# Kernel optimization log

Hardware: AMD Instinct MI355X
Metric: run time of the kernel (lower is better)

## Reference

```python
import jax, jax.numpy as jnp
import numpy as np

E, S, L, V, PMAX = 256, 64, 3, 256, 2000
DILATIONS = (1, 2, 4, 8)


def _layernorm(x, g, b, eps=1e-5):
    m = x.mean(-1, keepdims=True)
    v = ((x - m) ** 2).mean(-1, keepdims=True)
    return (x - m) * jax.lax.rsqrt(v + eps) * g + b


def _ssm_layer(x, in_w, conv_w, conv_b, dt_w, A_log, D_param, B_w, C_w, out_w, ln_g, ln_b):
    # x: [B, T, D]
    Bsz, T, Dm = x.shape
    xr = x @ in_w.T                                  # [B,T,2D]
    x_in, x_res = xr[..., :Dm], xr[..., Dm:]
    # causal depthwise conv, kernel=4, left-pad 3 (== torch pad=3 then [:, :, :T])
    xt = x_in.transpose(0, 2, 1)                     # [B,D,T]
    xc = jax.lax.conv_general_dilated(
        xt, conv_w[:, None, :], (1,), [(3, 0)],
        feature_group_count=Dm, dimension_numbers=('NCH', 'OIH', 'NCH'))
    xc = jax.nn.silu((xc + conv_b[None, :, None]).transpose(0, 2, 1))  # [B,T,D]
    A = -jnp.exp(A_log)                              # [D,S]
    Bm = xc @ B_w.T                                  # [B,T,S]
    Cm = xc @ C_w.T                                  # [B,T,S]
    dt = jax.nn.softplus(dt_w)                       # [D] per-channel timestep
    dA = 1.0 + dt[:, None] * A                       # Euler discretization I + dt*A, [D,S]
    h0 = jnp.zeros((Bsz, Dm, S), x.dtype)

    def step(h, inp):
        u_t, B_t, C_t = inp                          # [B,D],[B,S],[B,S]
        h = dA * h + (dt * u_t)[:, :, None] * B_t[:, None, :]   # [B,D,S]
        y = jnp.einsum('bs,bds->bd', C_t, h)
        return h, y

    _, ys = jax.lax.scan(step, h0, (xc.transpose(1, 0, 2), Bm.transpose(1, 0, 2), Cm.transpose(1, 0, 2)))
    y = ys.transpose(1, 0, 2) + D_param * xc         # [B,T,D]
    y = (y * jax.nn.silu(x_res)) @ out_w.T
    return _layernorm(y + x, ln_g, ln_b)


def _forward(tokens, tok_emb, pos_emb, in_w, conv_w, conv_b, dt_w, A_log, D_param,
             B_w, C_w, out_w, ln_g, ln_b, ctx_w, ctx_b, fus_w, fus_b, fus_ln_g, fus_ln_b):
    Bsz, T = tokens.shape
    x = tok_emb[tokens] + pos_emb[:T][None]          # [B,T,E]
    feats = x
    for i in range(L):
        feats = _ssm_layer(feats, in_w[i], conv_w[i], conv_b[i], dt_w[i], A_log[i],
                           D_param[i], B_w[i], C_w[i], out_w[i], ln_g[i], ln_b[i])
    # multi-dilation context convs on the raw embeddings
    xt = x.transpose(0, 2, 1)                        # [B,E,T]
    ctx = []
    for j, d in enumerate(DILATIONS):
        o = jax.lax.conv_general_dilated(
            xt, ctx_w[j], (1,), [(d, d)], rhs_dilation=(d,),
            dimension_numbers=('NCH', 'OIH', 'NCH'))
        ctx.append(o + ctx_b[j][None, :, None])
    ctx = jnp.concatenate(ctx, axis=1).transpose(0, 2, 1)      # [B,T,E]
    fused = jax.nn.relu(jnp.concatenate([feats, ctx], -1) @ fus_w.T + fus_b)
    return _layernorm(fused, fus_ln_g, fus_ln_b)


def setup_inputs() -> dict:
    key = jax.random.key(0)
    ks = jax.random.split(key, 16)
    Bsz, T = 32, 2000

    def n(k, shape, s):
        return jax.random.normal(k, shape, jnp.float32) * s

    return {
        'tokens': jax.random.randint(ks[0], (Bsz, T), 0, V),
        'tok_emb': n(ks[1], (V, E), 1.0),
        'pos_emb': n(ks[2], (PMAX, E), 1.0),
        'in_w': n(ks[3], (L, 2 * E, E), 0.05),
        'conv_w': n(ks[4], (L, E, 4), 0.2),
        'conv_b': jnp.zeros((L, E), jnp.float32),
        'dt_w': jax.random.uniform(ks[5], (L, E), jnp.float32, -0.01, 0.01),
        'A_log': jax.random.uniform(ks[6], (L, E, S), jnp.float32, -4.0, -1.0),
        'D_param': jnp.zeros((L, E), jnp.float32),
        'B_w': n(ks[7], (L, S, E), 0.05),
        'C_w': n(ks[8], (L, S, E), 0.05),
        'out_w': n(ks[9], (L, E, E), 0.05),
        'ln_g': jnp.ones((L, E), jnp.float32),
        'ln_b': jnp.zeros((L, E), jnp.float32),
        'ctx_w': n(ks[10], (4, E // 4, E, 3), 0.05),
        'ctx_b': jnp.zeros((4, E // 4), jnp.float32),
        'fus_w': n(ks[11], (E, 2 * E), 0.05),
        'fus_b': jnp.zeros((E,), jnp.float32),
        'fus_ln_g': jnp.ones((E,), jnp.float32),
        'fus_ln_b': jnp.zeros((E,), jnp.float32),
    }


def reference(tokens, tok_emb, pos_emb, in_w, conv_w, conv_b, dt_w, A_log, D_param,
              B_w, C_w, out_w, ln_g, ln_b, ctx_w, ctx_b, fus_w, fus_b, fus_ln_g, fus_ln_b):
    return _forward(tokens, tok_emb, pos_emb, in_w, conv_w, conv_b, dt_w, A_log, D_param,
                    B_w, C_w, out_w, ln_g, ln_b, ctx_w, ctx_b, fus_w, fus_b, fus_ln_g, fus_ln_b)
```

## Files before the change

### kernel.cpp

```cpp
#include <hip/hip_runtime.h>
#include <stdint.h>

#define B_ 32
#define T_ 2000
#define E_ 256
#define S_ 64
#define L_ 3
#define BT_ (B_*T_)
#define NC_ 25
#define CL_ 80
#define TS_ 16
#define NT_ (CL_/TS_)
#define TP_ (T_+16)

typedef short s8v __attribute__((ext_vector_type(8)));
typedef short s4v __attribute__((ext_vector_type(4)));
typedef float f4v __attribute__((ext_vector_type(4)));
typedef float f2v __attribute__((ext_vector_type(2)));
typedef unsigned short us;

__device__ __forceinline__ float b2f(us u){
    return __uint_as_float(((unsigned int)u) << 16);
}
__device__ __forceinline__ us f2b(float f){
    unsigned int x = __float_as_uint(f);
    x += 0x7fffu + ((x >> 16) & 1u);
    return (us)(x >> 16);
}

__global__ __launch_bounds__(256) void cvtw_k(const float* __restrict__ src,
    us* __restrict__ dst)
{
    int idx = blockIdx.x*256 + threadIdx.x;
    f4v v = *(const f4v*)(src + (size_t)idx*4);
    s4v o;
    #pragma unroll
    for (int j=0;j<4;j++) o[j] = (short)f2b(v[j]);
    *(s4v*)(dst + (size_t)idx*4) = o;
}

__global__ __launch_bounds__(256) void packbc_k(const float* __restrict__ Bw,
    const float* __restrict__ Cw, us* __restrict__ wbc)
{
    int idx = blockIdx.x*256 + threadIdx.x;
    int i = idx & 255; int r = (idx >> 8) & 127; int l = idx >> 15;
    const float* src = (r < 64) ? (Bw + ((size_t)l*S_ + r)*E_ + i)
                                : (Cw + ((size_t)l*S_ + (r-64))*E_ + i);
    wbc[idx] = f2b(*src);
}

__global__ __launch_bounds__(256) void packw_k(const float* __restrict__ cw,
    us* __restrict__ wp)
{
    int idx = blockIdx.x*256 + threadIdx.x;
    int i2 = idx % 768; int r = idx / 768;
    int c = r & 63; int j = r >> 6;
    int tap = i2 >> 8; int i = i2 & 255;
    wp[idx] = f2b(cw[(((size_t)(j*64 + c))*E_ + i)*3 + tap]);
}

__global__ __launch_bounds__(256) void embed_k(const int* __restrict__ tok,
    const float* __restrict__ te, const float* __restrict__ pe, us* __restrict__ x0)
{
    int idx = blockIdx.x*256 + threadIdx.x;
    int dg = idx & 31; int bt = idx >> 5; int t = bt % T_;
    int tk = tok[bt] & 255;
    const float* ta = te + (size_t)tk*E_ + dg*8;
    const float* pa = pe + (size_t)t*E_ + dg*8;
    f4v a0 = *(const f4v*)ta, a1 = *(const f4v*)(ta+4);
    f4v p0 = *(const f4v*)pa, p1 = *(const f4v*)(pa+4);
    s8v o;
    #pragma unroll
    for (int j=0;j<4;j++){
        o[j]   = (short)f2b(a0[j] + p0[j]);
        o[j+4] = (short)f2b(a1[j] + p1[j]);
    }
    *(s8v*)(x0 + (size_t)bt*E_ + dg*8) = o;
}

__global__ __launch_bounds__(256) void lconst_k(const float* __restrict__ dt_w,
    const float* __restrict__ A_log, float* __restrict__ dtv,
    float* __restrict__ dAT, float* __restrict__ dApT)
{
    int idx = blockIdx.x*256 + threadIdx.x;
    int d = idx & (E_-1); int s = idx >> 8;
    float dt = log1pf(expf(dt_w[d]));
    float A  = -expf(A_log[d*S_ + s]);
    float dA = 1.f + dt*A;
    dAT[s*E_ + d]  = dA;
    dApT[s*E_ + d] = powf(dA, (float)CL_);
    if (s == 0) dtv[d] = dt;
}

__global__ __launch_bounds__(256) void dwconv_k(const us* __restrict__ xin,
    const float* __restrict__ cw, const float* __restrict__ cb, us* __restrict__ xc)
{
    int idx = blockIdx.x*256 + threadIdx.x;
    int dg = idx & 31; int bt = idx >> 5; int t = bt % T_;
    int d0 = dg*8;
    float acc[8]; float w[8][4];
    #pragma unroll
    for (int j=0;j<8;j++){
        f4v wv = *(const f4v*)(cw + (size_t)(d0+j)*4);
        #pragma unroll
        for (int k=0;k<4;k++) w[j][k] = wv[k];
        acc[j] = cb[d0+j];
    }
    #pragma unroll
    for (int k=0;k<4;k++){
        if (t + k - 3 >= 0){
            s8v xv = *(const s8v*)(xin + (size_t)(bt + k - 3)*E_ + d0);
            #pragma unroll
            for (int j=0;j<8;j++) acc[j] = fmaf(b2f((us)xv[j]), w[j][k], acc[j]);
        }
    }
    s8v o;
    #pragma unroll
    for (int j=0;j<8;j++){ float v = acc[j]; v = v / (1.f + expf(-v)); o[j] = (short)f2b(v); }
    *(s8v*)(xc + (size_t)bt*E_ + d0) = o;
}

#define BM 128
#define BN 64
#define BK 32

template<int AMODE, int EPI>
__global__ __launch_bounds__(256)
void gemm_k(const us* __restrict__ A1, const us* __restrict__ A2,
            int lda, int shift,
            const us* __restrict__ W, int ldw,
            void* __restrict__ C1, const float* __restrict__ bias,
            int ldc, int K)
{
    __shared__ us Al[BM*BK];
    __shared__ us Bl[BN*BK];
    const int tid = threadIdx.x;
    const int wid = tid >> 6, lane = tid & 63;
    const int m0 = blockIdx.x * BM;
    const int n0 = blockIdx.y * BN;
    const int wr = wid >> 1, wc = wid & 1;
    f4v acc[4][2];
    #pragma unroll
    for (int a=0;a<4;a++)
        #pragma unroll
        for (int b=0;b<2;b++) acc[a][b] = (f4v){0.f,0.f,0.f,0.f};

    for (int k0 = 0; k0 < K; k0 += BK){
        s8v va[2], vb;
        #pragma unroll
        for (int i=0;i<2;i++){
            int g = i*256 + tid;
            int row = g >> 2, ks = g & 3;
            const us* src;
            if constexpr (AMODE==0){
                src = A1 + (size_t)(m0+row)*lda + k0 + ks*8;
            } else if constexpr (AMODE==2){
                int kk = k0 + ks*8;
                const us* base = (kk < E_) ? A1 : A2;
                src = base + (size_t)(m0+row)*E_ + (kk & (E_-1));
            } else {
                int kk = k0 + ks*8;
                int tap = kk >> 8; int kin = kk & (E_-1);
                int m = m0 + row; int bb = m / T_; int tt = m - bb*T_;
                src = A1 + ((size_t)bb*TP_ + 8 + tt + (tap-1)*shift)*E_ + kin;
            }
            va[i] = *(const s8v*)src;
        }
        {
            int row = tid >> 2, ks = tid & 3;
            vb = *(const s8v*)(W + (size_t)(n0+row)*ldw + k0 + ks*8);
        }
        if (k0) __syncthreads();
        #pragma unroll
        for (int i=0;i<2;i++) *(s8v*)(Al + (size_t)(i*256 + tid)*8) = va[i];
        *(s8v*)(Bl + (size_t)tid*8) = vb;
        __syncthreads();

        s8v af[4], bfr[2];
        #pragma unroll
        for (int mr=0;mr<4;mr++)
            af[mr] = *(const s8v*)(Al + ((size_t)(wr*64 + mr*16 + (lane&15))*4 + (lane>>4))*8);
        #pragma unroll
        for (int nr=0;nr<2;nr++)
            bfr[nr] = *(const s8v*)(Bl + ((size_t)(wc*32 + nr*16 + (lane&15))*4 + (lane>>4))*8);
        #pragma unroll
        for (int mr=0;mr<4;mr++)
            #pragma unroll
            for (int nr=0;nr<2;nr++)
                acc[mr][nr] = __builtin_amdgcn_mfma_f32_16x16x32_bf16(af[mr], bfr[nr], acc[mr][nr], 0, 0, 0);
    }
    #pragma unroll
    for (int mr=0;mr<4;mr++){
        #pragma unroll
        for (int nr=0;nr<2;nr++){
            int col = n0 + wc*32 + nr*16 + (lane & 15);
            int rb  = m0 + wr*64 + mr*16 + ((lane >> 4) << 2);
            #pragma unroll
            for (int i=0;i<4;i++){
                float val = acc[mr][nr][i];
                size_t row = (size_t)(rb + i);
                if constexpr (EPI==0){
                    ((us*)C1)[row*ldc + col] = f2b(val);
                } else if constexpr (EPI==2){
                    ((float*)C1)[row*ldc + col] = val;
                } else if constexpr (EPI==5){
                    val += bias[col];
                    ((us*)C1)[row*ldc + col] = f2b(val);
                } else {
                    val += bias[col];
                    val = fmaxf(val, 0.f);
                    ((float*)C1)[row*ldc + col] = val;
                }
            }
        }
    }
}

__global__ __launch_bounds__(1024) void scan_h(
    const float* __restrict__ dAT, const float* __restrict__ dtv,
    const us* __restrict__ xc, const float* __restrict__ BC,
    us* __restrict__ H)
{
    __shared__ float sBC[TS_*128];
    __shared__ us    sXC[TS_*256];
    int b = blockIdx.x / NC_, c = blockIdx.x % NC_;
    int tid = threadIdx.x;
    int d = tid >> 2, sg = tid & 3, s0 = sg*16;
    f4v h4[4], dA4[4];
    #pragma unroll
    for (int q=0;q<4;q++){
        #pragma unroll
        for (int j=0;j<4;j++){ h4[q][j] = 0.f; dA4[q][j] = dAT[(s0+q*4+j)*E_ + d]; }
    }
    float dtd = dtv[d];
    int t0 = c*CL_;
    size_t base0 = (size_t)b*T_ + t0;
    *(f2v*)(&sBC[tid*2]) = *(const f2v*)(BC + base0*128 + tid*2);
    *(s4v*)(&sXC[tid*4]) = *(const s4v*)(xc + base0*E_ + tid*4);
    __syncthreads();
    for (int tile = 0; tile < NT_; ++tile){
        f2v pv; s4v pxv;
        bool more = (tile+1 < NT_);
        if (more){
            size_t basen = base0 + (size_t)(tile+1)*TS_;
            pv  = *(const f2v*)(BC + basen*128 + tid*2);
            pxv = *(const s4v*)(xc + basen*E_ + tid*4);
        }
        for (int st = 0; st < TS_; ++st){
            float u = dtd * b2f(sXC[st*256 + d]);
            const f4v* Bp = (const f4v*)(&sBC[st*128 + s0]);
            #pragma unroll
            for (int q=0;q<4;q++) h4[q] = dA4[q]*h4[q] + Bp[q]*u;
        }
        __syncthreads();
        if (more){
            *(f2v*)(&sBC[tid*2]) = pv;
            *(s4v*)(&sXC[tid*4]) = pxv;
        }
        __syncthreads();
    }
    size_t hb = ((size_t)(b*NC_ + c))*S_*E_ + d;
    #pragma unroll
    for (int q=0;q<4;q++)
        #pragma unroll
        for (int j=0;j<4;j++) H[hb + (size_t)(s0+q*4+j)*E_] = f2b(h4[q][j]);
}

__global__ __launch_bounds__(256) void carry_k(const float* __restrict__ dApT,
    us* H)
{
    int idx = blockIdx.x*256 + threadIdx.x;
    int d = idx & (E_-1); int s = (idx >> 8) & (S_-1); int b = idx >> 14;
    float ap = dApT[s*E_ + d];
    size_t base = ((size_t)(b*NC_))*S_*E_ + (size_t)s*E_ + d;
    float hh = 0.f;
    for (int c=0;c<NC_;c++){
        size_t p = base + (size_t)c*S_*E_;
        float hl = b2f(H[p]);
        H[p] = f2b(hh);
        hh = fmaf(ap, hh, hl);
    }
}

__global__ __launch_bounds__(1024) void scan_y(
    const float* __restrict__ dAT, const float* __restrict__ dtv,
    const us* __restrict__ xc, const float* __restrict__ BC,
    const us* __restrict__ Hc, us* __restrict__ ys)
{
    __shared__ float sBC[TS_*128];
    __shared__ us    sXC[TS_*256];
    int b = blockIdx.x / NC_, c = blockIdx.x % NC_;
    int tid = threadIdx.x;
    int d = tid >> 2, sg = tid & 3, s0 = sg*16;
    f4v h4[4], dA4[4];
    size_t cb = ((size_t)(b*NC_ + c))*S_*E_ + d;
    #pragma unroll
    for (int q=0;q<4;q++){
        #pragma unroll
        for (int j=0;j<4;j++){
            int s = s0 + q*4 + j;
            dA4[q][j] = dAT[s*E_ + d];
            h4[q][j]  = b2f(Hc[cb + (size_t)s*E_]);
        }
    }
    float dtd = dtv[d];
    int t0 = c*CL_;
    size_t base0 = (size_t)b*T_ + t0;
    *(f2v*)(&sBC[tid*2]) = *(const f2v*)(BC + base0*128 + tid*2);
    *(s4v*)(&sXC[tid*4]) = *(const s4v*)(xc + base0*E_ + tid*4);
    __syncthreads();
    for (int tile = 0; tile < NT_; ++tile){
        f2v pv; s4v pxv;
        bool more = (tile+1 < NT_);
        if (more){
            size_t basen = base0 + (size_t)(tile+1)*TS_;
            pv  = *(const f2v*)(BC + basen*128 + tid*2);
            pxv = *(const s4v*)(xc + basen*E_ + tid*4);
        }
        for (int st = 0; st < TS_; ++st){
            int t = t0 + tile*TS_ + st;
            float u = dtd * b2f(sXC[st*256 + d]);
            const f4v* Bp = (const f4v*)(&sBC[st*128 + s0]);
            const f4v* Cp = (const f4v*)(&sBC[st*128 + 64 + s0]);
            f4v y4 = (f4v){0.f,0.f,0.f,0.f};
            #pragma unroll
            for (int q=0;q<4;q++){
                h4[q] = dA4[q]*h4[q] + Bp[q]*u;
                y4    = y4 + Cp[q]*h4[q];
            }
            float y = (y4[0]+y4[1]) + (y4[2]+y4[3]);
            y += __shfl_xor(y, 1, 64);
            y += __shfl_xor(y, 2, 64);
            if (sg == 0) ys[((size_t)b*T_ + t)*E_ + d] = f2b(y);
        }
        __syncthreads();
        if (more){
            *(f2v*)(&sBC[tid*2]) = pv;
            *(s4v*)(&sXC[tid*4]) = pxv;
        }
        __syncthreads();
    }
}

__global__ __launch_bounds__(256) void zin_k(const us* __restrict__ ys,
    const us* xc, const us* __restrict__ xres,
    const float* __restrict__ Dp, us* zout)
{
    size_t e0 = ((size_t)blockIdx.x*256 + threadIdx.x)*4;
    int d0 = (int)(e0 & (E_-1));
    s4v yv  = *(const s4v*)(ys + e0);
    s4v xcv = *(const s4v*)(xc + e0);
    s4v xrv = *(const s4v*)(xres + e0);
    f4v dv  = *(const f4v*)(Dp + d0);
    s4v o;
    #pragma unroll
    for (int j=0;j<4;j++){
        float y  = b2f((us)yv[j]) + dv[j] * b2f((us)xcv[j]);
        float xr = b2f((us)xrv[j]);
        o[j] = (short)f2b(y * (xr / (1.f + expf(-xr))));
    }
    *(s4v*)(zout + e0) = o;
}

__global__ __launch_bounds__(256) void ln_k(const us* z,
    const us* __restrict__ resid, const float* __restrict__ g,
    const float* __restrict__ bb, us* out)
{
    int wid = threadIdx.x >> 6, lane = threadIdx.x & 63;
    size_t row = (size_t)blockIdx.x*4 + wid;
    size_t base = row*E_ + lane*4;
    s4v zv = *(const s4v*)(z + base);
    float v[4];
    #pragma unroll
    for (int j=0;j<4;j++) v[j] = b2f((us)zv[j]);
    if (resid){
        s4v rv = *(const s4v*)(resid + base);
        #pragma unroll
        for (int j=0;j<4;j++) v[j] += b2f((us)rv[j]);
    }
    float sum = v[0]+v[1]+v[2]+v[3];
    float sq  = v[0]*v[0]+v[1]*v[1]+v[2]*v[2]+v[3]*v[3];
    #pragma unroll
    for (int off=32; off>0; off>>=1){
        sum += __shfl_xor(sum, off, 64);
        sq  += __shfl_xor(sq,  off, 64);
    }
    float mean = sum * (1.f/E_);
    float var  = sq * (1.f/E_) - mean*mean;
    float rstd = rsqrtf(var + 1e-5f);
    f4v gv = *(const f4v*)(g + lane*4);
    f4v bv = *(const f4v*)(bb + lane*4);
    s4v o;
    #pragma unroll
    for (int j=0;j<4;j++)
        o[j] = (short)f2b((v[j]-mean)*rstd*gv[j] + bv[j]);
    *(s4v*)(out + base) = o;
}

__global__ __launch_bounds__(256) void ln_f32_k(const float* z,
    const float* __restrict__ g, const float* __restrict__ bb, float* out)
{
    int wid = threadIdx.x >> 6, lane = threadIdx.x & 63;
    size_t row = (size_t)blockIdx.x*4 + wid;
    size_t base = row*E_ + lane*4;
    f4v v = *(const f4v*)(z + base);
    float sum = v[0]+v[1]+v[2]+v[3];
    float sq  = v[0]*v[0]+v[1]*v[1]+v[2]*v[2]+v[3]*v[3];
    #pragma unroll
    for (int off=32; off>0; off>>=1){
        sum += __shfl_xor(sum, off, 64);
        sq  += __shfl_xor(sq,  off, 64);
    }
    float mean = sum * (1.f/E_);
    float var  = sq * (1.f/E_) - mean*mean;
    float rstd = rsqrtf(var + 1e-5f);
    f4v gv = *(const f4v*)(g + lane*4);
    f4v bv = *(const f4v*)(bb + lane*4);
    f4v o;
    #pragma unroll
    for (int j=0;j<4;j++)
        o[j] = (v[j]-mean)*rstd*gv[j] + bv[j];
    *(f4v*)(out + base) = o;
}

__global__ __launch_bounds__(256) void xpad_k(const us* __restrict__ x0,
    us* __restrict__ xp)
{
    int idx = blockIdx.x*256 + threadIdx.x;
    int dg = idx & 31; int r = idx >> 5;
    int tp = r % TP_; int b = r / TP_;
    s8v o;
    if (tp < 8 || tp >= T_+8){
        #pragma unroll
        for (int j=0;j<8;j++) o[j] = 0;
    } else {
        o = *(const s8v*)(x0 + ((size_t)b*T_ + tp - 8)*E_ + dg*8);
    }
    *(s8v*)(xp + (size_t)r*E_ + dg*8) = o;
}

__global__ void probe_k(const unsigned int* __restrict__ outw,
    const us* p0, const us* p1, float* outf)
{
    if (threadIdx.x | blockIdx.x) return;
    bool zero = true;
    for (int i=0;i<512 && zero;i++)              if (outw[i]) zero = false;
    for (int i=2000000;i<2000512 && zero;i++)    if (outw[i]) zero = false;
    if (!zero) return;
    int code = 256, f;
    f=0; for (int i=0;i<256;i++) if (p0[i] & 0x7FFF) f=1;  code += 128*f;
    f=0; for (int i=0;i<256;i++) if (p1[i] & 0x7FFF) f=1;  code += 16*f;
    outf[0] = (float)code;
}

extern "C" void kernel_launch(void* const* d_in, const int* in_sizes, int n_in,
                              void* d_out, int out_size, void* d_ws, size_t ws_size,
                              hipStream_t stream)
{
    const int*   tokens   = (const int*)d_in[0];
    const float* tok_emb  = (const float*)d_in[1];
    const float* pos_emb  = (const float*)d_in[2];
    const float* in_w     = (const float*)d_in[3];
    const float* conv_w   = (const float*)d_in[4];
    const float* conv_b   = (const float*)d_in[5];
    const float* dt_w     = (const float*)d_in[6];
    const float* A_log    = (const float*)d_in[7];
    const float* D_param  = (const float*)d_in[8];
    const float* B_w      = (const float*)d_in[9];
    const float* C_w      = (const float*)d_in[10];
    const float* out_w    = (const float*)d_in[11];
    const float* ln_g     = (const float*)d_in[12];
    const float* ln_b     = (const float*)d_in[13];
    const float* ctx_w    = (const float*)d_in[14];
    const float* ctx_b    = (const float*)d_in[15];
    const float* fus_w    = (const float*)d_in[16];
    const float* fus_b    = (const float*)d_in[17];
    const float* fus_ln_g = (const float*)d_in[18];
    const float* fus_ln_b = (const float*)d_in[19];

    char* ws = (char*)d_ws;
    size_t off = 0;
    auto alloc = [&](size_t bytes){ size_t o = off; off += (bytes + 255) & ~(size_t)255; return o; };
    const size_t BT = BT_;
    size_t o_p0  = alloc(BT*E_*2);
    size_t o_p1  = alloc(BT*E_*2);
    size_t o_ctx = alloc(BT*E_*2);
    size_t o_xin = alloc(BT*E_*2);
    size_t o_xc  = alloc(BT*E_*2);
    size_t o_bc  = alloc(BT*128*4);
    size_t o_h   = alloc((size_t)B_*NC_*S_*E_*2);
    size_t o_wp  = alloc((size_t)4*64*768*2);
    size_t o_wi  = alloc((size_t)L_*2*E_*E_*2);
    size_t o_wo  = alloc((size_t)L_*E_*E_*2);
    size_t o_wbc = alloc((size_t)L_*128*E_*2);
    size_t o_wf  = alloc((size_t)E_*2*E_*2);
    size_t o_dtv = alloc(E_*4);
    size_t o_dat = alloc(E_*S_*4);
    size_t o_dap = alloc(E_*S_*4);
    (void)ws_size; (void)in_sizes; (void)n_in; (void)out_size;

    us* P0   = (us*)(ws + o_p0);
    us* P1   = (us*)(ws + o_p1);
    us* CTXB = (us*)(ws + o_ctx);
    us* XIN  = (us*)(ws + o_xin);
    us* XC   = (us*)(ws + o_xc);
    float* BCf = (float*)(ws + o_bc);
    us* Hb   = (us*)(ws + o_h);
    us* WP   = (us*)(ws + o_wp);
    us* WI   = (us*)(ws + o_wi);
    us* WO   = (us*)(ws + o_wo);
    us* WBC  = (us*)(ws + o_wbc);
    us* WF   = (us*)(ws + o_wf);
    float* DTV  = (float*)(ws + o_dtv);
    float* DAT  = (float*)(ws + o_dat);
    float* DAPT = (float*)(ws + o_dap);
    us* XPAD = XIN;
    us* YS   = (us*)d_out;

    cvtw_k<<<L_*2*E_*E_/1024, 256, 0, stream>>>(in_w,  WI);
    cvtw_k<<<L_*E_*E_/1024,   256, 0, stream>>>(out_w, WO);
    cvtw_k<<<E_*2*E_/1024,    256, 0, stream>>>(fus_w, WF);
    packbc_k<<<L_*128*E_/256, 256, 0, stream>>>(B_w, C_w, WBC);
    packw_k<<<4*64*768/256,   256, 0, stream>>>(ctx_w, WP);

    embed_k<<<BT_*32/256, 256, 0, stream>>>(tokens, tok_emb, pos_emb, P0);

    xpad_k<<<B_*TP_*32/256, 256, 0, stream>>>(P0, XPAD);
    const int dil[4] = {1,2,4,8};
    for (int j = 0; j < 4; ++j){
        gemm_k<3,5><<<dim3(BT_/BM, 1), 256, 0, stream>>>(
            XPAD, nullptr, E_, dil[j], WP + (size_t)j*64*768, 768,
            CTXB + j*64, ctx_b + j*64, E_, 768);
    }

    for (int l = 0; l < L_; ++l){
        const us* xprev = (l==1) ? P1 : P0;
        us*       xnext = (l==1) ? P0 : P1;

        lconst_k<<<E_*S_/256, 256, 0, stream>>>(dt_w + (size_t)l*E_, A_log + (size_t)l*E_*S_,
                                                DTV, DAT, DAPT);
        gemm_k<0,0><<<dim3(BT_/BM, E_/BN), 256, 0, stream>>>(
            xprev, nullptr, E_, 0, WI + (size_t)l*2*E_*E_, E_, XIN, nullptr, E_, E_);
        dwconv_k<<<BT_*32/256, 256, 0, stream>>>(XIN, conv_w + (size_t)l*E_*4, conv_b + (size_t)l*E_, XC);
        gemm_k<0,0><<<dim3(BT_/BM, E_/BN), 256, 0, stream>>>(
            xprev, nullptr, E_, 0, WI + (size_t)l*2*E_*E_ + (size_t)E_*E_, E_, XIN , nullptr, E_, E_);
        gemm_k<0,2><<<dim3(BT_/BM, 2), 256, 0, stream>>>(
            XC, nullptr, E_, 0, WBC + (size_t)l*128*E_, E_, BCf, nullptr, 128, E_);
        scan_h<<<B_*NC_, 1024, 0, stream>>>(DAT, DTV, XC, BCf, Hb);
        carry_k<<<B_*S_*E_/256, 256, 0, stream>>>(DAPT, Hb);
        scan_y<<<B_*NC_, 1024, 0, stream>>>(DAT, DTV, XC, BCf, Hb, YS);
        zin_k<<<BT_*E_/4/256, 256, 0, stream>>>(YS, XC, XIN, D_param + (size_t)l*E_, XC );
        gemm_k<0,0><<<dim3(BT_/BM, E_/BN), 256, 0, stream>>>(
            XC, nullptr, E_, 0, WO + (size_t)l*E_*E_, E_, XIN , nullptr, E_, E_);
        ln_k<<<BT_/4, 256, 0, stream>>>(XIN, xprev, ln_g + (size_t)l*E_, ln_b + (size_t)l*E_, xnext);
    }

    gemm_k<2,6><<<dim3(BT_/BM, E_/BN), 256, 0, stream>>>(
        P1, CTXB, E_, 0, WF, 2*E_, d_out, fus_b, E_, 2*E_);
    ln_f32_k<<<BT_/4, 256, 0, stream>>>((const float*)d_out, fus_ln_g, fus_ln_b, (float*)d_out);

    probe_k<<<1, 64, 0, stream>>>((const unsigned int*)d_out, P0, P1, (float*)d_out);
}
```

Before: 1.463 ms.

## Store B/C projections as bf16 and double-buffer scan shared memory

The B/C projection GEMM now writes bf16 instead of fp32, which halves the BC buffer. The two scan kernels read that packed bf16 and unpack even/odd state lanes with bit shifts. The scans also double-buffer their shared-memory tiles, dropping one __syncthreads per tile, and fully unroll the inner timestep loop. This is meant to cut memory traffic and synchronisation in the scan, at the cost of bf16 rounding of B and C and more registers per thread.

```diff
diff --git a/kernel.cpp b/kernel.cpp
--- a/kernel.cpp
+++ b/kernel.cpp
@@ -16,7 +16,6 @@
 typedef short s8v __attribute__((ext_vector_type(8)));
 typedef short s4v __attribute__((ext_vector_type(4)));
 typedef float f4v __attribute__((ext_vector_type(4)));
-typedef float f2v __attribute__((ext_vector_type(2)));
 typedef unsigned short us;
 
 __device__ __forceinline__ float b2f(us u){
@@ -218,52 +217,62 @@
 
 __global__ __launch_bounds__(1024) void scan_h(
     const float* __restrict__ dAT, const float* __restrict__ dtv,
-    const us* __restrict__ xc, const float* __restrict__ BC,
+    const us* __restrict__ xc, const us* __restrict__ BC,
     us* __restrict__ H)
 {
-    __shared__ float sBC[TS_*128];
-    __shared__ us    sXC[TS_*256];
+    __shared__ us sB[2][TS_*64];
+    __shared__ us sXC[2][TS_*256];
     int b = blockIdx.x / NC_, c = blockIdx.x % NC_;
     int tid = threadIdx.x;
     int d = tid >> 2, sg = tid & 3, s0 = sg*16;
-    f4v h4[4], dA4[4];
-    #pragma unroll
-    for (int q=0;q<4;q++){
-        #pragma unroll
-        for (int j=0;j<4;j++){ h4[q][j] = 0.f; dA4[q][j] = dAT[(s0+q*4+j)*E_ + d]; }
+    float hE[8], hO[8], dAE[8], dAO[8];
+    #pragma unroll
+    for (int k=0;k<8;k++){
+        int se = s0 + 2*k;
+        dAE[k] = dAT[se*E_ + d]; dAO[k] = dAT[(se+1)*E_ + d];
+        hE[k] = 0.f; hO[k] = 0.f;
     }
     float dtd = dtv[d];
     int t0 = c*CL_;
-    size_t base0 = (size_t)b*T_ + t0;
-    *(f2v*)(&sBC[tid*2]) = *(const f2v*)(BC + base0*128 + tid*2);
-    *(s4v*)(&sXC[tid*4]) = *(const s4v*)(xc + base0*E_ + tid*4);
+    size_t gBC = ((size_t)b*T_ + t0)*128;
+    size_t gXC = ((size_t)b*T_ + t0)*E_;
+    sB[0][tid] = BC[gBC + (size_t)(tid>>6)*128 + (tid & 63)];
+    *(s4v*)&sXC[0][tid*4] = *(const s4v*)(xc + gXC + tid*4);
     __syncthreads();
+    int cur = 0;
     for (int tile = 0; tile < NT_; ++tile){
-        f2v pv; s4v pxv;
+        us pB; s4v pXC;
         bool more = (tile+1 < NT_);
         if (more){
-            size_t basen = base0 + (size_t)(tile+1)*TS_;
-            pv  = *(const f2v*)(BC + basen*128 + tid*2);
-            pxv = *(const s4v*)(xc + basen*E_ + tid*4);
-        }
+            size_t o = (size_t)(tile+1)*TS_;
+            pB  = BC[gBC + (o + (size_t)(tid>>6))*128 + (tid & 63)];
+            pXC = *(const s4v*)(xc + gXC + o*E_ + tid*4);
+        }
+        #pragma unroll
         for (int st = 0; st < TS_; ++st){
-            float u = dtd * b2f(sXC[st*256 + d]);
-            const f4v* Bp = (const f4v*)(&sBC[st*128 + s0]);
+            float u = dtd * b2f(sXC[cur][st*256 + d]);
+            const unsigned int* Bw = (const unsigned int*)&sB[cur][st*64 + s0];
             #pragma unroll
-            for (int q=0;q<4;q++) h4[q] = dA4[q]*h4[q] + Bp[q]*u;
+            for (int k=0;k<8;k++){
+                unsigned int bw = Bw[k];
+                hE[k] = fmaf(dAE[k], hE[k], u*__uint_as_float(bw << 16));
+                hO[k] = fmaf(dAO[k], hO[k], u*__uint_as_float(bw & 0xffff0000u));
+            }
+        }
+        if (more){
+            sB[cur^1][tid] = pB;
+            *(s4v*)&sXC[cur^1][tid*4] = pXC;
         }
         __syncthreads();
-        if (more){
-            *(f2v*)(&sBC[tid*2]) = pv;
-            *(s4v*)(&sXC[tid*4]) = pxv;
-        }
-        __syncthreads();
+        cur ^= 1;
     }
     size_t hb = ((size_t)(b*NC_ + c))*S_*E_ + d;
     #pragma unroll
-    for (int q=0;q<4;q++)
-        #pragma unroll
-        for (int j=0;j<4;j++) H[hb + (size_t)(s0+q*4+j)*E_] = f2b(h4[q][j]);
+    for (int k=0;k<8;k++){
+        int se = s0 + 2*k;
+        H[hb + (size_t)se*E_]     = f2b(hE[k]);
+        H[hb + (size_t)(se+1)*E_] = f2b(hO[k]);
+    }
 }
 
 __global__ __launch_bounds__(256) void carry_k(const float* __restrict__ dApT,
@@ -284,61 +293,63 @@
 
 __global__ __launch_bounds__(1024) void scan_y(
     const float* __restrict__ dAT, const float* __restrict__ dtv,
-    const us* __restrict__ xc, const float* __restrict__ BC,
+    const us* __restrict__ xc, const us* __restrict__ BC,
     const us* __restrict__ Hc, us* __restrict__ ys)
 {
-    __shared__ float sBC[TS_*128];
-    __shared__ us    sXC[TS_*256];
+    __shared__ us sBC[2][TS_*128];
+    __shared__ us sXC[2][TS_*256];
     int b = blockIdx.x / NC_, c = blockIdx.x % NC_;
     int tid = threadIdx.x;
     int d = tid >> 2, sg = tid & 3, s0 = sg*16;
-    f4v h4[4], dA4[4];
+    float hE[8], hO[8], dAE[8], dAO[8];
     size_t cb = ((size_t)(b*NC_ + c))*S_*E_ + d;
     #pragma unroll
-    for (int q=0;q<4;q++){
-        #pragma unroll
-        for (int j=0;j<4;j++){
-            int s = s0 + q*4 + j;
-            dA4[q][j] = dAT[s*E_ + d];
-            h4[q][j]  = b2f(Hc[cb + (size_t)s*E_]);
-        }
+    for (int k=0;k<8;k++){
+        int se = s0 + 2*k;
+        dAE[k] = dAT[se*E_ + d];     dAO[k] = dAT[(se+1)*E_ + d];
+        hE[k]  = b2f(Hc[cb + (size_t)se*E_]);
+        hO[k]  = b2f(Hc[cb + (size_t)(se+1)*E_]);
     }
     float dtd = dtv[d];
     int t0 = c*CL_;
-    size_t base0 = (size_t)b*T_ + t0;
-    *(f2v*)(&sBC[tid*2]) = *(const f2v*)(BC + base0*128 + tid*2);
-    *(s4v*)(&sXC[tid*4]) = *(const s4v*)(xc + base0*E_ + tid*4);
+    size_t gBC = ((size_t)b*T_ + t0)*128;
+    size_t gXC = ((size_t)b*T_ + t0)*E_;
+    *(unsigned int*)&sBC[0][tid*2] = *(const unsigned int*)(BC + gBC + tid*2);
+    *(s4v*)&sXC[0][tid*4] = *(const s4v*)(xc + gXC + tid*4);
     __syncthreads();
+    int cur = 0;
     for (int tile = 0; tile < NT_; ++tile){
-        f2v pv; s4v pxv;
+        unsigned int pBC; s4v pXC;
         bool more = (tile+1 < NT_);
         if (more){
-            size_t basen = base0 + (size_t)(tile+1)*TS_;
-            pv  = *(const f2v*)(BC + basen*128 + tid*2);
-            pxv = *(const s4v*)(xc + basen*E_ + tid*4);
-        }
+            size_t o = (size_t)(tile+1)*TS_;
+            pBC = *(const unsigned int*)(BC + gBC + o*128 + tid*2);
+            pXC = *(const s4v*)(xc + gXC + o*E_ + tid*4);
+        }
+        #pragma unroll
         for (int st = 0; st < TS_; ++st){
-            int t = t0 + tile*TS_ + st;
-            float u = dtd * b2f(sXC[st*256 + d]);
-            const f4v* Bp = (const f4v*)(&sBC[st*128 + s0]);
-            const f4v* Cp = (const f4v*)(&sBC[st*128 + 64 + s0]);
-            f4v y4 = (f4v){0.f,0.f,0.f,0.f};
+            float u = dtd * b2f(sXC[cur][st*256 + d]);
+            const unsigned int* Bw = (const unsigned int*)&sBC[cur][st*128 + s0];
+            const unsigned int* Cw = (const unsigned int*)&sBC[cur][st*128 + 64 + s0];
+            float y = 0.f;
             #pragma unroll
-            for (int q=0;q<4;q++){
-                h4[q] = dA4[q]*h4[q] + Bp[q]*u;
-                y4    = y4 + Cp[q]*h4[q];
+            for (int k=0;k<8;k++){
+                unsigned int bw = Bw[k], cw = Cw[k];
+                hE[k] = fmaf(dAE[k], hE[k], u*__uint_as_float(bw << 16));
+                hO[k] = fmaf(dAO[k], hO[k], u*__uint_as_float(bw & 0xffff0000u));
+                y = fmaf(__uint_as_float(cw << 16),        hE[k], y);
+                y = fmaf(__uint_as_float(cw & 0xffff0000u), hO[k], y);
             }
-            float y = (y4[0]+y4[1]) + (y4[2]+y4[3]);
-            y += __shfl_xor(y, 1, 64);
-            y += __shfl_xor(y, 2, 64);
-            if (sg == 0) ys[((size_t)b*T_ + t)*E_ + d] = f2b(y);
+            y += __shfl_xor(y, 1, 4);
+            y += __shfl_xor(y, 2, 4);
+            if (sg == 0) ys[gXC + (size_t)(tile*TS_ + st)*E_ + d] = f2b(y);
+        }
+        if (more){
+            *(unsigned int*)&sBC[cur^1][tid*2] = pBC;
+            *(s4v*)&sXC[cur^1][tid*4] = pXC;
         }
         __syncthreads();
-        if (more){
-            *(f2v*)(&sBC[tid*2]) = pv;
-            *(s4v*)(&sXC[tid*4]) = pxv;
-        }
-        __syncthreads();
+        cur ^= 1;
     }
 }
 
@@ -487,7 +498,7 @@
     size_t o_ctx = alloc(BT*E_*2);
     size_t o_xin = alloc(BT*E_*2);
     size_t o_xc  = alloc(BT*E_*2);
-    size_t o_bc  = alloc(BT*128*4);
+    size_t o_bc  = alloc(BT*128*2);
     size_t o_h   = alloc((size_t)B_*NC_*S_*E_*2);
     size_t o_wp  = alloc((size_t)4*64*768*2);
     size_t o_wi  = alloc((size_t)L_*2*E_*E_*2);
@@ -504,7 +515,7 @@
     us* CTXB = (us*)(ws + o_ctx);
     us* XIN  = (us*)(ws + o_xin);
     us* XC   = (us*)(ws + o_xc);
-    float* BCf = (float*)(ws + o_bc);
+    us* BCb  = (us*)(ws + o_bc);
     us* Hb   = (us*)(ws + o_h);
     us* WP   = (us*)(ws + o_wp);
     us* WI   = (us*)(ws + o_wi);
@@ -544,11 +555,11 @@
         dwconv_k<<<BT_*32/256, 256, 0, stream>>>(XIN, conv_w + (size_t)l*E_*4, conv_b + (size_t)l*E_, XC);
         gemm_k<0,0><<<dim3(BT_/BM, E_/BN), 256, 0, stream>>>(
             xprev, nullptr, E_, 0, WI + (size_t)l*2*E_*E_ + (size_t)E_*E_, E_, XIN , nullptr, E_, E_);
-        gemm_k<0,2><<<dim3(BT_/BM, 2), 256, 0, stream>>>(
-            XC, nullptr, E_, 0, WBC + (size_t)l*128*E_, E_, BCf, nullptr, 128, E_);
-        scan_h<<<B_*NC_, 1024, 0, stream>>>(DAT, DTV, XC, BCf, Hb);
+        gemm_k<0,0><<<dim3(BT_/BM, 2), 256, 0, stream>>>(
+            XC, nullptr, E_, 0, WBC + (size_t)l*128*E_, E_, BCb, nullptr, 128, E_);
+        scan_h<<<B_*NC_, 1024, 0, stream>>>(DAT, DTV, XC, BCb, Hb);
         carry_k<<<B_*S_*E_/256, 256, 0, stream>>>(DAPT, Hb);
-        scan_y<<<B_*NC_, 1024, 0, stream>>>(DAT, DTV, XC, BCf, Hb, YS);
+        scan_y<<<B_*NC_, 1024, 0, stream>>>(DAT, DTV, XC, BCb, Hb, YS);
         zin_k<<<BT_*E_/4/256, 256, 0, stream>>>(YS, XC, XIN, D_param + (size_t)l*E_, XC );
         gemm_k<0,0><<<dim3(BT_/BM, E_/BN), 256, 0, stream>>>(
             XC, nullptr, E_, 0, WO + (size_t)l*E_*E_, E_, XIN , nullptr, E_, E_);
```

Result: slower. 2.608 ms (+78.3%).

## Load GEMM tiles directly into LDS and merge in_proj GEMMs

Applied to the files above, without the earlier changes.

The GEMM kernel now uses global_load_lds to copy A and B tiles straight from global memory into shared memory. This replaces the load-to-register then store-to-LDS staging and moves the barrier to the top of the K loop. The two per-layer in_proj GEMMs (x_in and x_res halves) become one launch with twice the N-blocks. A new epilogue mode splits its output columns into XIN and a new XRES buffer placed in the unused upper half of the output buffer, and zin_k reads x_res from there. This saves a launch and a second pass over the input activations per layer, but it depends on the direct-to-LDS path being correctly synchronized and on the output buffer being large enough to hold the scratch region.

```diff
diff --git a/kernel.cpp b/kernel.cpp
--- a/kernel.cpp
+++ b/kernel.cpp
@@ -129,7 +129,8 @@
 void gemm_k(const us* __restrict__ A1, const us* __restrict__ A2,
             int lda, int shift,
             const us* __restrict__ W, int ldw,
-            void* __restrict__ C1, const float* __restrict__ bias,
+            void* __restrict__ C1, void* __restrict__ C2,
+            const float* __restrict__ bias,
             int ldc, int K)
 {
     __shared__ us Al[BM*BK];
@@ -146,7 +147,7 @@
         for (int b=0;b<2;b++) acc[a][b] = (f4v){0.f,0.f,0.f,0.f};
 
     for (int k0 = 0; k0 < K; k0 += BK){
-        s8v va[2], vb;
+        if (k0) __syncthreads();
         #pragma unroll
         for (int i=0;i<2;i++){
             int g = i*256 + tid;
@@ -164,16 +165,17 @@
                 int m = m0 + row; int bb = m / T_; int tt = m - bb*T_;
                 src = A1 + ((size_t)bb*TP_ + 8 + tt + (tap-1)*shift)*E_ + kin;
             }
-            va[i] = *(const s8v*)src;
+            __builtin_amdgcn_global_load_lds(
+                (const __attribute__((address_space(1))) void*)src,
+                (__attribute__((address_space(3))) void*)(Al + (size_t)g*8), 16, 0, 0);
         }
         {
             int row = tid >> 2, ks = tid & 3;
-            vb = *(const s8v*)(W + (size_t)(n0+row)*ldw + k0 + ks*8);
-        }
-        if (k0) __syncthreads();
-        #pragma unroll
-        for (int i=0;i<2;i++) *(s8v*)(Al + (size_t)(i*256 + tid)*8) = va[i];
-        *(s8v*)(Bl + (size_t)tid*8) = vb;
+            const us* src = W + (size_t)(n0+row)*ldw + k0 + ks*8;
+            __builtin_amdgcn_global_load_lds(
+                (const __attribute__((address_space(1))) void*)src,
+                (__attribute__((address_space(3))) void*)(Bl + (size_t)tid*8), 16, 0, 0);
+        }
         __syncthreads();
 
         s8v af[4], bfr[2];
@@ -201,6 +203,9 @@
                 size_t row = (size_t)(rb + i);
                 if constexpr (EPI==0){
                     ((us*)C1)[row*ldc + col] = f2b(val);
+                } else if constexpr (EPI==1){
+                    if (col < E_) ((us*)C1)[row*E_ + col] = f2b(val);
+                    else          ((us*)C2)[row*E_ + (col - E_)] = f2b(val);
                 } else if constexpr (EPI==2){
                     ((float*)C1)[row*ldc + col] = val;
                 } else if constexpr (EPI==5){
@@ -516,6 +521,7 @@
     float* DAPT = (float*)(ws + o_dap);
     us* XPAD = XIN;
     us* YS   = (us*)d_out;
+    us* XRES = (us*)d_out + BT*E_;
 
     cvtw_k<<<L_*2*E_*E_/1024, 256, 0, stream>>>(in_w,  WI);
     cvtw_k<<<L_*E_*E_/1024,   256, 0, stream>>>(out_w, WO);
@@ -530,7 +536,7 @@
     for (int j = 0; j < 4; ++j){
         gemm_k<3,5><<<dim3(BT_/BM, 1), 256, 0, stream>>>(
             XPAD, nullptr, E_, dil[j], WP + (size_t)j*64*768, 768,
-            CTXB + j*64, ctx_b + j*64, E_, 768);
+            CTXB + j*64, nullptr, ctx_b + j*64, E_, 768);
     }
 
     for (int l = 0; l < L_; ++l){
@@ -539,24 +545,22 @@
 
         lconst_k<<<E_*S_/256, 256, 0, stream>>>(dt_w + (size_t)l*E_, A_log + (size_t)l*E_*S_,
                                                 DTV, DAT, DAPT);
-        gemm_k<0,0><<<dim3(BT_/BM, E_/BN), 256, 0, stream>>>(
-            xprev, nullptr, E_, 0, WI + (size_t)l*2*E_*E_, E_, XIN, nullptr, E_, E_);
+        gemm_k<0,1><<<dim3(BT_/BM, 2*E_/BN), 256, 0, stream>>>(
+            xprev, nullptr, E_, 0, WI + (size_t)l*2*E_*E_, E_, XIN, XRES, nullptr, E_, E_);
         dwconv_k<<<BT_*32/256, 256, 0, stream>>>(XIN, conv_w + (size_t)l*E_*4, conv_b + (size_t)l*E_, XC);
-        gemm_k<0,0><<<dim3(BT_/BM, E_/BN), 256, 0, stream>>>(
-            xprev, nullptr, E_, 0, WI + (size_t)l*2*E_*E_ + (size_t)E_*E_, E_, XIN , nullptr, E_, E_);
         gemm_k<0,2><<<dim3(BT_/BM, 2), 256, 0, stream>>>(
-            XC, nullptr, E_, 0, WBC + (size_t)l*128*E_, E_, BCf, nullptr, 128, E_);
+            XC, nullptr, E_, 0, WBC + (size_t)l*128*E_, E_, BCf, nullptr, nullptr, 128, E_);
         scan_h<<<B_*NC_, 1024, 0, stream>>>(DAT, DTV, XC, BCf, Hb);
         carry_k<<<B_*S_*E_/256, 256, 0, stream>>>(DAPT, Hb);
         scan_y<<<B_*NC_, 1024, 0, stream>>>(DAT, DTV, XC, BCf, Hb, YS);
-        zin_k<<<BT_*E_/4/256, 256, 0, stream>>>(YS, XC, XIN, D_param + (size_t)l*E_, XC );
+        zin_k<<<BT_*E_/4/256, 256, 0, stream>>>(YS, XC, XRES, D_param + (size_t)l*E_, XC );
         gemm_k<0,0><<<dim3(BT_/BM, E_/BN), 256, 0, stream>>>(
-            XC, nullptr, E_, 0, WO + (size_t)l*E_*E_, E_, XIN , nullptr, E_, E_);
+            XC, nullptr, E_, 0, WO + (size_t)l*E_*E_, E_, XIN , nullptr, nullptr, E_, E_);
         ln_k<<<BT_/4, 256, 0, stream>>>(XIN, xprev, ln_g + (size_t)l*E_, ln_b + (size_t)l*E_, xnext);
     }
 
     gemm_k<2,6><<<dim3(BT_/BM, E_/BN), 256, 0, stream>>>(
-        P1, CTXB, E_, 0, WF, 2*E_, d_out, fus_b, E_, 2*E_);
+        P1, CTXB, E_, 0, WF, 2*E_, d_out, nullptr, fus_b, E_, 2*E_);
     ln_f32_k<<<BT_/4, 256, 0, stream>>>((const float*)d_out, fus_ln_g, fus_ln_b, (float*)d_out);
 
     probe_k<<<1, 64, 0, stream>>>((const unsigned int*)d_out, P0, P1, (float*)d_out);
```

After: 1.467 ms. No clear change (+0.3%).
